# Performance work log

Measured on AMD Instinct MI355X. Metric: run time of the kernel, lower is better.

The kernel has to match this reference:

```python
import jax, jax.numpy as jnp
import numpy as np

N = 100_000   # nodes
E = 1_600_000 # edges
F = 16        # input node features
H = 32        # embedding_size
B = 256       # graphs in batch


def setup_inputs() -> dict:
    key = jax.random.key(0)
    ks = jax.random.split(key, 13)
    s = 0.1  # small init scale for weights
    return {
        "x": jax.random.normal(ks[0], (N, F), jnp.float32),
        "edge_index": jax.random.randint(ks[1], (2, E), 0, N, dtype=jnp.int64),
        "batch_index": jnp.sort(jax.random.randint(ks[2], (N,), 0, B, dtype=jnp.int64)),
        "W0": jax.random.normal(ks[3], (F, H), jnp.float32) * s,
        "b0": jax.random.normal(ks[4], (H,), jnp.float32) * s,
        "W1": jax.random.normal(ks[5], (H, H), jnp.float32) * s,
        "b1": jax.random.normal(ks[6], (H,), jnp.float32) * s,
        "W2": jax.random.normal(ks[7], (H, H), jnp.float32) * s,
        "b2": jax.random.normal(ks[8], (H,), jnp.float32) * s,
        "W3": jax.random.normal(ks[9], (H, H), jnp.float32) * s,
        "b3": jax.random.normal(ks[10], (H, H), jnp.float32)[:, 0] * s,
        "W_out": jax.random.normal(ks[11], (3 * H, 1), jnp.float32) * s,
        "b_out": jax.random.normal(ks[12], (1,), jnp.float32) * s,
    }


def _gcn_forward(x, edge_index, batch_index,
                 W0, b0, W1, b1, W2, b2, W3, b3, W_out, b_out):
    src, dst = edge_index[0], edge_index[1]
    n = x.shape[0]
    # GCN symmetric normalization with self-loops: deg includes the +1 self-loop
    deg = jax.ops.segment_sum(jnp.ones(src.shape[0], x.dtype), dst, num_segments=n) + 1.0
    dinv = jax.lax.rsqrt(deg)
    edge_coef = (dinv[src] * dinv[dst])[:, None]   # [E,1]
    self_coef = (dinv * dinv)[:, None]             # [N,1]

    def conv(h, W, b):
        # x' = D^{-1/2}(A+I)D^{-1/2} (h W) + b  (PyG GCNConv)
        hW = h @ W
        agg = jax.ops.segment_sum(hW[src] * edge_coef, dst, num_segments=n)
        agg = agg + hW * self_coef  # self-loop contribution
        return agg + b

    h = jnp.tanh(conv(x, W0, b0))
    h = jnp.tanh(conv(h, W1, b1))
    h = jnp.tanh(conv(h, W2, b2))
    h = jnp.tanh(conv(h, W3, b3))

    # Global max / mean / add pooling over batch_index
    gmax = jax.ops.segment_max(h, batch_index, num_segments=B)
    gsum = jax.ops.segment_sum(h, batch_index, num_segments=B)
    cnt = jax.ops.segment_sum(jnp.ones(n, h.dtype), batch_index, num_segments=B)
    gmean = gsum / jnp.maximum(cnt, 1.0)[:, None]
    pooled = jnp.concatenate([gmax, gmean, gsum], axis=1)  # [B, 3H]

    out = pooled @ W_out + b_out  # [B, 1]
    return out, pooled


def reference(x, edge_index, batch_index,
              W0, b0, W1, b1, W2, b2, W3, b3, W_out, b_out):
    return _gcn_forward(x, edge_index, batch_index,
                        W0, b0, W1, b1, W2, b2, W3, b3, W_out, b_out)
```

## Files before the change

kernel.cpp:

```cpp
#include <hip/hip_runtime.h>
#include <math.h>

#define N_NODES 100000
#define N_EDGES 1600000
#define F_IN    16
#define H_DIM   32
#define B_GRAPHS 256

#define BSHIFT  7
#define BSIZE   128
#define NBUCKET ((N_NODES + BSIZE - 1) / BSIZE)
#define EPB     8192
#define NCHUNK  ((N_EDGES + EPB - 1) / EPB)
#define CAPB    2560
#define CSTRIDE 2944
#define TPAD    (NBUCKET * CSTRIDE)
#define CURSTR  16
#define NPB     16
#define LAYER_BLOCKS (N_NODES / NPB)

__device__ inline float bf_lo(unsigned u) { return __uint_as_float(u << 16); }
__device__ inline float bf_hi(unsigned u) { return __uint_as_float(u & 0xffff0000u); }
__device__ inline unsigned pack_bf16x2(float a, float b) {
    unsigned ua = __float_as_uint(a), ub = __float_as_uint(b);
    ua += 0x7fffu + ((ua >> 16) & 1u);
    ub += 0x7fffu + ((ub >> 16) & 1u);
    return (ua >> 16) | (ub & 0xffff0000u);
}

__global__ __launch_bounds__(256) void init_cur_kernel(int* __restrict__ bucket_cur) {
    int b = blockIdx.x * 256 + threadIdx.x;
    if (b < NBUCKET) bucket_cur[b * CURSTR] = b * CAPB;
}

__global__ __launch_bounds__(1024) void passB_kernel(const int* __restrict__ ei,
                                                     int* __restrict__ bucket_cur,
                                                     unsigned* __restrict__ rec_out) {
    __shared__ int hist[NBUCKET];
    __shared__ int gcur[NBUCKET];
    int t = threadIdx.x;
    for (int k = t; k < NBUCKET; k += 1024) hist[k] = 0;
    __syncthreads();

    const int* dst = ei + N_EDGES;
    int base = blockIdx.x * EPB;
    int end  = base + EPB; if (end > N_EDGES) end = N_EDGES;

    for (int e = base + t; e < end; e += 1024) atomicAdd(&hist[dst[e] >> BSHIFT], 1);
    __syncthreads();

    for (int k = t; k < NBUCKET; k += 1024) {
        int h = hist[k];
        gcur[k] = h ? atomicAdd(&bucket_cur[k * CURSTR], h) : 0;
    }
    __syncthreads();

    for (int e = base + t; e < end; e += 1024) {
        int d = dst[e], s = ei[e];
        int bk = d >> BSHIFT;
        int pos = atomicAdd(&gcur[bk], 1);
        rec_out[pos] = (unsigned)s | ((unsigned)(d & (BSIZE - 1)) << 20);
    }
}

__global__ __launch_bounds__(256) void dinv_kernel(const unsigned* __restrict__ rec,
                                                   const int* __restrict__ bucket_cur,
                                                   float* __restrict__ dinv) {
    __shared__ int cnt[BSIZE];
    int t = threadIdx.x, b = blockIdx.x;
    if (t < BSIZE) cnt[t] = 0;
    __syncthreads();
    int e1 = bucket_cur[b * CURSTR];
    for (int e = b * CAPB + t; e < e1; e += 256) atomicAdd(&cnt[rec[e] >> 20], 1);
    __syncthreads();
    int nd = (b << BSHIFT) + t;
    if (t < BSIZE && nd < N_NODES) dinv[nd] = rsqrtf((float)cnt[t] + 1.0f);
}

__global__ __launch_bounds__(256) void passC_kernel(const unsigned* __restrict__ rec,
                                                    const int* __restrict__ bucket_cur,
                                                    const float* __restrict__ dinv,
                                                    int2* __restrict__ row_meta,
                                                    int2* __restrict__ csr) {
    __shared__ unsigned stage[CAPB];
    __shared__ int cnt[BSIZE];
    __shared__ int pds[BSIZE];
    __shared__ int cur[BSIZE];
    __shared__ float sdv[BSIZE];
    int t = threadIdx.x, b = blockIdx.x;
    int node0 = b << BSHIFT;
    int e0 = b * CAPB;
    int n = bucket_cur[b * CURSTR] - e0;
    int pbase = b * CSTRIDE;
    if (t < BSIZE) {
        cnt[t] = 0;
        int nd = node0 + t;
        sdv[t] = (nd < N_NODES) ? dinv[nd] : 0.f;
    }
    __syncthreads();
    for (int k = t; k < n; k += 256) {
        unsigned r = rec[e0 + k];
        stage[k] = r;
        atomicAdd(&cnt[r >> 20], 1);
    }
    __syncthreads();
    int pd = 0;
    if (t < BSIZE) { pd = (cnt[t] + 3) & ~3; pds[t] = pd; }
    __syncthreads();
    for (int off = 1; off < BSIZE; off <<= 1) {
        int v = (t < BSIZE && t >= off) ? pds[t - off] : 0;
        __syncthreads();
        if (t < BSIZE) pds[t] += v;
        __syncthreads();
    }
    if (t < BSIZE) {
        int startp = pbase + pds[t] - pd;
        cur[t] = startp;
        int nd = node0 + t;
        if (nd < N_NODES) {
            row_meta[nd] = make_int2(startp, pd);
            for (int k = startp + cnt[t]; k < startp + pd; ++k)
                csr[k] = make_int2(nd, 0);
        }
    }
    __syncthreads();
    for (int k = t; k < n; k += 256) {
        unsigned r = stage[k];
        int dl = r >> 20;
        int s  = r & 0xFFFFF;
        int pos = atomicAdd(&cur[dl], 1);
        csr[pos] = make_int2(s, __float_as_int(dinv[s] * sdv[dl]));
    }
}

template <int FIN, bool PACKED>
__global__ __launch_bounds__(256) void layer_kernel(
        const void* __restrict__ h_in_v,
        const int2* __restrict__ row_meta,
        const int4* __restrict__ csr4,
        const float* __restrict__ dinv,
        const float* __restrict__ W,
        const float* __restrict__ bias,
        unsigned* __restrict__ h_out) {
    constexpr int STR = FIN + 1;
    __shared__ float sW[FIN * H_DIM];
    __shared__ float sb[H_DIM];
    __shared__ float agg[NPB][STR];
    int t = threadIdx.x;
    for (int k = t; k < FIN * H_DIM; k += 256) sW[k] = W[k];
    if (t < H_DIM) sb[t] = bias[t];

    int nl = t >> 4, ln = t & 15;
    int i = blockIdx.x * NPB + nl;
    int2 m = row_meta[i];
    float di = dinv[i], di2 = di * di;
    int q    = m.x >> 1;
    int qend = (m.x + m.y) >> 1;

    if (PACKED) {
        const unsigned* hp = (const unsigned*)h_in_v;
        unsigned u = hp[i * 16 + ln];
        float acc0 = bf_lo(u) * di2, acc1 = bf_hi(u) * di2;
        for (; q + 8 <= qend; q += 8) {
            int4 ca[8];
#pragma unroll
            for (int k = 0; k < 8; ++k) ca[k] = csr4[q + k];
            unsigned v[16];
#pragma unroll
            for (int k = 0; k < 8; ++k) {
                v[2 * k]     = hp[ca[k].x * 16 + ln];
                v[2 * k + 1] = hp[ca[k].z * 16 + ln];
            }
#pragma unroll
            for (int k = 0; k < 8; ++k) {
                float c0 = __int_as_float(ca[k].y), c1 = __int_as_float(ca[k].w);
                acc0 += bf_lo(v[2 * k]) * c0 + bf_lo(v[2 * k + 1]) * c1;
                acc1 += bf_hi(v[2 * k]) * c0 + bf_hi(v[2 * k + 1]) * c1;
            }
        }
        if (q + 4 <= qend) {
            int4 ca[4];
#pragma unroll
            for (int k = 0; k < 4; ++k) ca[k] = csr4[q + k];
#pragma unroll
            for (int k = 0; k < 4; ++k) {
                unsigned v0 = hp[ca[k].x * 16 + ln], v1 = hp[ca[k].z * 16 + ln];
                float c0 = __int_as_float(ca[k].y), c1 = __int_as_float(ca[k].w);
                acc0 += bf_lo(v0) * c0 + bf_lo(v1) * c1;
                acc1 += bf_hi(v0) * c0 + bf_hi(v1) * c1;
            }
            q += 4;
        }
        if (q < qend) {
            int4 a = csr4[q], b = csr4[q + 1];
            unsigned v0 = hp[a.x * 16 + ln], v1 = hp[a.z * 16 + ln];
            unsigned v2 = hp[b.x * 16 + ln], v3 = hp[b.z * 16 + ln];
            float c0 = __int_as_float(a.y), c1 = __int_as_float(a.w);
            float c2 = __int_as_float(b.y), c3 = __int_as_float(b.w);
            acc0 += bf_lo(v0) * c0 + bf_lo(v1) * c1 + bf_lo(v2) * c2 + bf_lo(v3) * c3;
            acc1 += bf_hi(v0) * c0 + bf_hi(v1) * c1 + bf_hi(v2) * c2 + bf_hi(v3) * c3;
        }
        agg[nl][2 * ln]     = acc0;
        agg[nl][2 * ln + 1] = acc1;
    } else {
        const float* xf = (const float*)h_in_v;
        float acc = xf[i * F_IN + ln] * di2;
        for (; q + 8 <= qend; q += 8) {
            int4 ca[8];
#pragma unroll
            for (int k = 0; k < 8; ++k) ca[k] = csr4[q + k];
            float v[16];
#pragma unroll
            for (int k = 0; k < 8; ++k) {
                v[2 * k]     = xf[ca[k].x * F_IN + ln];
                v[2 * k + 1] = xf[ca[k].z * F_IN + ln];
            }
#pragma unroll
            for (int k = 0; k < 8; ++k)
                acc += v[2 * k] * __int_as_float(ca[k].y)
                     + v[2 * k + 1] * __int_as_float(ca[k].w);
        }
        if (q + 4 <= qend) {
            int4 ca[4];
#pragma unroll
            for (int k = 0; k < 4; ++k) ca[k] = csr4[q + k];
#pragma unroll
            for (int k = 0; k < 4; ++k)
                acc += xf[ca[k].x * F_IN + ln] * __int_as_float(ca[k].y)
                     + xf[ca[k].z * F_IN + ln] * __int_as_float(ca[k].w);
            q += 4;
        }
        if (q < qend) {
            int4 a = csr4[q], b = csr4[q + 1];
            acc += xf[a.x * F_IN + ln] * __int_as_float(a.y)
                 + xf[a.z * F_IN + ln] * __int_as_float(a.w)
                 + xf[b.x * F_IN + ln] * __int_as_float(b.y)
                 + xf[b.z * F_IN + ln] * __int_as_float(b.w);
        }
        agg[nl][ln] = acc;
    }
    __syncthreads();

    int j0 = 2 * ln;
    float o0 = sb[j0], o1 = sb[j0 + 1];
    const float* arow = &agg[nl][0];
#pragma unroll
    for (int k = 0; k < FIN; ++k) {
        float a = arow[k];
        o0 += a * sW[k * H_DIM + j0];
        o1 += a * sW[k * H_DIM + j0 + 1];
    }
    h_out[i * 16 + ln] = pack_bf16x2(tanhf(o0), tanhf(o1));
}

__global__ __launch_bounds__(256) void pool_kernel(const unsigned* __restrict__ hp,
                                                   const int* __restrict__ batch,
                                                   const float* __restrict__ Wout,
                                                   const float* __restrict__ bout,
                                                   float* __restrict__ out) {
    int b = blockIdx.x;
    int t = threadIdx.x;
    int lane_n = t >> 5;
    int j = t & 31;

    int lo = 0, hi = N_NODES;
    while (lo < hi) { int mid = (lo + hi) >> 1; if (batch[mid] < b) lo = mid + 1; else hi = mid; }
    int start = lo;
    hi = N_NODES;
    while (lo < hi) { int mid = (lo + hi) >> 1; if (batch[mid] < b + 1) lo = mid + 1; else hi = mid; }
    int end = lo;

    float vmax = -INFINITY, vsum = 0.f;
    for (int i = start + lane_n; i < end; i += 8) {
        unsigned q = hp[i * 16 + (j >> 1)];
        float v = (j & 1) ? bf_hi(q) : bf_lo(q);
        vmax = fmaxf(vmax, v);
        vsum += v;
    }

    __shared__ float smax[8][32];
    __shared__ float ssum[8][32];
    __shared__ float pool96[96];
    smax[lane_n][j] = vmax;
    ssum[lane_n][j] = vsum;
    __syncthreads();

    if (t < 32) {
        float m = smax[0][t], s = ssum[0][t];
#pragma unroll
        for (int n = 1; n < 8; ++n) { m = fmaxf(m, smax[n][t]); s += ssum[n][t]; }
        int cnt = end - start;
        float mean = s / fmaxf((float)cnt, 1.0f);
        pool96[t]      = m;
        pool96[32 + t] = mean;
        pool96[64 + t] = s;
    }
    __syncthreads();

    if (t < 96) out[B_GRAPHS + b * 96 + t] = pool96[t];

    __shared__ float dotbuf[96];
    if (t < 96) dotbuf[t] = pool96[t] * Wout[t];
    __syncthreads();
    if (t == 0) {
        float acc = 0.f;
#pragma unroll
        for (int k = 0; k < 96; ++k) acc += dotbuf[k];
        out[b] = acc + bout[0];
    }
}

extern "C" void kernel_launch(void* const* d_in, const int* in_sizes, int n_in,
                              void* d_out, int out_size, void* d_ws, size_t ws_size,
                              hipStream_t stream) {
    const float* x     = (const float*)d_in[0];
    const int*   ei    = (const int*)  d_in[1];
    const int*   batch = (const int*)  d_in[2];
    const float* W0    = (const float*)d_in[3];
    const float* b0    = (const float*)d_in[4];
    const float* W1    = (const float*)d_in[5];
    const float* b1    = (const float*)d_in[6];
    const float* W2    = (const float*)d_in[7];
    const float* b2    = (const float*)d_in[8];
    const float* W3    = (const float*)d_in[9];
    const float* b3    = (const float*)d_in[10];
    const float* Wout  = (const float*)d_in[11];
    const float* bout  = (const float*)d_in[12];
    float* out = (float*)d_out;

    char* p = (char*)d_ws;
    float*    dinv       = (float*)p;    p += (size_t)N_NODES * 4;
    unsigned* hA         = (unsigned*)p; p += (size_t)N_NODES * 16 * 4;
    unsigned* rec        = (unsigned*)p; p += (size_t)NBUCKET * CAPB * 4;
    int2*     csr        = (int2*)p;     p += (size_t)TPAD * 8;
    int2*     row_meta   = (int2*)p;     p += (size_t)N_NODES * 8;
    int*      bucket_cur = (int*)p;      p += (size_t)NBUCKET * CURSTR * 4;
    unsigned* hB = rec;

    init_cur_kernel<<<(NBUCKET + 255) / 256, 256, 0, stream>>>(bucket_cur);
    passB_kernel<<<NCHUNK, 1024, 0, stream>>>(ei, bucket_cur, rec);
    dinv_kernel<<<NBUCKET, 256, 0, stream>>>(rec, bucket_cur, dinv);
    passC_kernel<<<NBUCKET, 256, 0, stream>>>(rec, bucket_cur, dinv, row_meta, csr);

    layer_kernel<F_IN, false><<<LAYER_BLOCKS, 256, 0, stream>>>(
        x,  row_meta, (const int4*)csr, dinv, W0, b0, hA);
    layer_kernel<H_DIM, true><<<LAYER_BLOCKS, 256, 0, stream>>>(
        hA, row_meta, (const int4*)csr, dinv, W1, b1, hB);
    layer_kernel<H_DIM, true><<<LAYER_BLOCKS, 256, 0, stream>>>(
        hB, row_meta, (const int4*)csr, dinv, W2, b2, hA);
    layer_kernel<H_DIM, true><<<LAYER_BLOCKS, 256, 0, stream>>>(
        hA, row_meta, (const int4*)csr, dinv, W3, b3, hB);

    pool_kernel<<<B_GRAPHS, 256, 0, stream>>>(hB, batch, Wout, bout, out);
}
```

Baseline: 261.5 us.

## Fuse pooling into last GCN layer and compute degrees via global atomics

Removes the separate dinv kernel by counting in-degrees with global atomics during edge bucketing and computing rsqrt inline in passC. The last layer now reduces each 16-node block's tanh outputs per graph in shared memory and pushes max (via order-preserving uint encoding), sum and count to global atomics. A tiny single-block head kernel then finishes mean, writes the pooled output and does the output dot product. This cuts a kernel launch, the binary searches and the pool re-read of h, in exchange for 1.6M extra global atomics on deg and atomic contention on per-graph accumulators, with non-deterministic float sum order.

```diff
diff --git a/kernel.cpp b/kernel.cpp
--- a/kernel.cpp
+++ b/kernel.cpp
@@ -27,15 +27,31 @@
     ub += 0x7fffu + ((ub >> 16) & 1u);
     return (ua >> 16) | (ub & 0xffff0000u);
 }
-
-__global__ __launch_bounds__(256) void init_cur_kernel(int* __restrict__ bucket_cur) {
-    int b = blockIdx.x * 256 + threadIdx.x;
-    if (b < NBUCKET) bucket_cur[b * CURSTR] = b * CAPB;
+__device__ inline unsigned fenc(float f) {
+    unsigned u = __float_as_uint(f);
+    return (u & 0x80000000u) ? ~u : (u | 0x80000000u);
+}
+__device__ inline float fdec(unsigned k) {
+    if (k == 0u) return -INFINITY;
+    return __uint_as_float((k & 0x80000000u) ? (k ^ 0x80000000u) : ~k);
+}
+
+__global__ __launch_bounds__(256) void init_kernel(int* __restrict__ bucket_cur,
+                                                   int* __restrict__ deg,
+                                                   unsigned* __restrict__ gmaxk,
+                                                   float* __restrict__ gsum,
+                                                   int* __restrict__ gcnt) {
+    int t = blockIdx.x * 256 + threadIdx.x;
+    if (t < NBUCKET) bucket_cur[t * CURSTR] = t * CAPB;
+    if (t < N_NODES) deg[t] = 0;
+    if (t < B_GRAPHS * H_DIM) { gmaxk[t] = 0u; gsum[t] = 0.f; }
+    if (t < B_GRAPHS) gcnt[t] = 0;
 }
 
 __global__ __launch_bounds__(1024) void passB_kernel(const int* __restrict__ ei,
                                                      int* __restrict__ bucket_cur,
-                                                     unsigned* __restrict__ rec_out) {
+                                                     unsigned* __restrict__ rec_out,
+                                                     int* __restrict__ deg) {
     __shared__ int hist[NBUCKET];
     __shared__ int gcur[NBUCKET];
     int t = threadIdx.x;
@@ -46,7 +62,11 @@
     int base = blockIdx.x * EPB;
     int end  = base + EPB; if (end > N_EDGES) end = N_EDGES;
 
-    for (int e = base + t; e < end; e += 1024) atomicAdd(&hist[dst[e] >> BSHIFT], 1);
+    for (int e = base + t; e < end; e += 1024) {
+        int d = dst[e];
+        atomicAdd(&hist[d >> BSHIFT], 1);
+        atomicAdd(&deg[d], 1);
+    }
     __syncthreads();
 
     for (int k = t; k < NBUCKET; k += 1024) {
@@ -63,25 +83,12 @@
     }
 }
 
-__global__ __launch_bounds__(256) void dinv_kernel(const unsigned* __restrict__ rec,
-                                                   const int* __restrict__ bucket_cur,
-                                                   float* __restrict__ dinv) {
-    __shared__ int cnt[BSIZE];
-    int t = threadIdx.x, b = blockIdx.x;
-    if (t < BSIZE) cnt[t] = 0;
-    __syncthreads();
-    int e1 = bucket_cur[b * CURSTR];
-    for (int e = b * CAPB + t; e < e1; e += 256) atomicAdd(&cnt[rec[e] >> 20], 1);
-    __syncthreads();
-    int nd = (b << BSHIFT) + t;
-    if (t < BSIZE && nd < N_NODES) dinv[nd] = rsqrtf((float)cnt[t] + 1.0f);
-}
-
 __global__ __launch_bounds__(256) void passC_kernel(const unsigned* __restrict__ rec,
                                                     const int* __restrict__ bucket_cur,
-                                                    const float* __restrict__ dinv,
+                                                    const int* __restrict__ deg,
                                                     int2* __restrict__ row_meta,
-                                                    int2* __restrict__ csr) {
+                                                    int2* __restrict__ csr,
+                                                    float* __restrict__ dinv) {
     __shared__ unsigned stage[CAPB];
     __shared__ int cnt[BSIZE];
     __shared__ int pds[BSIZE];
@@ -95,7 +102,7 @@
     if (t < BSIZE) {
         cnt[t] = 0;
         int nd = node0 + t;
-        sdv[t] = (nd < N_NODES) ? dinv[nd] : 0.f;
+        sdv[t] = (nd < N_NODES) ? rsqrtf((float)deg[nd] + 1.0f) : 0.f;
     }
     __syncthreads();
     for (int k = t; k < n; k += 256) {
@@ -119,6 +126,7 @@
         int nd = node0 + t;
         if (nd < N_NODES) {
             row_meta[nd] = make_int2(startp, pd);
+            dinv[nd] = sdv[t];
             for (int k = startp + cnt[t]; k < startp + pd; ++k)
                 csr[k] = make_int2(nd, 0);
         }
@@ -129,11 +137,12 @@
         int dl = r >> 20;
         int s  = r & 0xFFFFF;
         int pos = atomicAdd(&cur[dl], 1);
-        csr[pos] = make_int2(s, __float_as_int(dinv[s] * sdv[dl]));
-    }
-}
-
-template <int FIN, bool PACKED>
+        float ds = rsqrtf((float)deg[s] + 1.0f);
+        csr[pos] = make_int2(s, __float_as_int(ds * sdv[dl]));
+    }
+}
+
+template <int FIN, bool PACKED, bool POOL>
 __global__ __launch_bounds__(256) void layer_kernel(
         const void* __restrict__ h_in_v,
         const int2* __restrict__ row_meta,
@@ -141,11 +150,16 @@
         const float* __restrict__ dinv,
         const float* __restrict__ W,
         const float* __restrict__ bias,
-        unsigned* __restrict__ h_out) {
+        unsigned* __restrict__ h_out,
+        const int* __restrict__ batch,
+        unsigned* __restrict__ gmaxk,
+        float* __restrict__ gsum,
+        int* __restrict__ gcnt) {
     constexpr int STR = FIN + 1;
     __shared__ float sW[FIN * H_DIM];
     __shared__ float sb[H_DIM];
     __shared__ float agg[NPB][STR];
+    __shared__ int sg[NPB];
     int t = threadIdx.x;
     for (int k = t; k < FIN * H_DIM; k += 256) sW[k] = W[k];
     if (t < H_DIM) sb[t] = bias[t];
@@ -250,64 +264,63 @@
         o0 += a * sW[k * H_DIM + j0];
         o1 += a * sW[k * H_DIM + j0 + 1];
     }
-    h_out[i * 16 + ln] = pack_bf16x2(tanhf(o0), tanhf(o1));
-}
-
-__global__ __launch_bounds__(256) void pool_kernel(const unsigned* __restrict__ hp,
-                                                   const int* __restrict__ batch,
+    float t0 = tanhf(o0), t1 = tanhf(o1);
+
+    if (!POOL) {
+        h_out[i * 16 + ln] = pack_bf16x2(t0, t1);
+    } else {
+        __syncthreads();
+        agg[nl][j0]     = t0;
+        agg[nl][j0 + 1] = t1;
+        if (t < NPB) sg[t] = batch[blockIdx.x * NPB + t];
+        __syncthreads();
+        if (t < H_DIM) {
+            int j = t;
+            int g = sg[0];
+            float mx = agg[0][j], sm = mx;
+            int run = 1;
+            for (int nn = 1; nn < NPB; ++nn) {
+                float v = agg[nn][j];
+                if (sg[nn] != g) {
+                    atomicMax(&gmaxk[g * H_DIM + j], fenc(mx));
+                    atomicAdd(&gsum[g * H_DIM + j], sm);
+                    if (j == 0) atomicAdd(&gcnt[g], run);
+                    g = sg[nn]; mx = v; sm = v; run = 1;
+                } else {
+                    mx = fmaxf(mx, v); sm += v; ++run;
+                }
+            }
+            atomicMax(&gmaxk[g * H_DIM + j], fenc(mx));
+            atomicAdd(&gsum[g * H_DIM + j], sm);
+            if (j == 0) atomicAdd(&gcnt[g], run);
+        }
+    }
+}
+
+__global__ __launch_bounds__(256) void head_kernel(const unsigned* __restrict__ gmaxk,
+                                                   const float* __restrict__ gsum,
+                                                   const int* __restrict__ gcnt,
                                                    const float* __restrict__ Wout,
                                                    const float* __restrict__ bout,
                                                    float* __restrict__ out) {
-    int b = blockIdx.x;
-    int t = threadIdx.x;
-    int lane_n = t >> 5;
-    int j = t & 31;
-
-    int lo = 0, hi = N_NODES;
-    while (lo < hi) { int mid = (lo + hi) >> 1; if (batch[mid] < b) lo = mid + 1; else hi = mid; }
-    int start = lo;
-    hi = N_NODES;
-    while (lo < hi) { int mid = (lo + hi) >> 1; if (batch[mid] < b + 1) lo = mid + 1; else hi = mid; }
-    int end = lo;
-
-    float vmax = -INFINITY, vsum = 0.f;
-    for (int i = start + lane_n; i < end; i += 8) {
-        unsigned q = hp[i * 16 + (j >> 1)];
-        float v = (j & 1) ? bf_hi(q) : bf_lo(q);
-        vmax = fmaxf(vmax, v);
-        vsum += v;
-    }
-
-    __shared__ float smax[8][32];
-    __shared__ float ssum[8][32];
-    __shared__ float pool96[96];
-    smax[lane_n][j] = vmax;
-    ssum[lane_n][j] = vsum;
-    __syncthreads();
-
-    if (t < 32) {
-        float m = smax[0][t], s = ssum[0][t];
-#pragma unroll
-        for (int n = 1; n < 8; ++n) { m = fmaxf(m, smax[n][t]); s += ssum[n][t]; }
-        int cnt = end - start;
-        float mean = s / fmaxf((float)cnt, 1.0f);
-        pool96[t]      = m;
-        pool96[32 + t] = mean;
-        pool96[64 + t] = s;
-    }
-    __syncthreads();
-
-    if (t < 96) out[B_GRAPHS + b * 96 + t] = pool96[t];
-
-    __shared__ float dotbuf[96];
-    if (t < 96) dotbuf[t] = pool96[t] * Wout[t];
-    __syncthreads();
-    if (t == 0) {
-        float acc = 0.f;
-#pragma unroll
-        for (int k = 0; k < 96; ++k) acc += dotbuf[k];
-        out[b] = acc + bout[0];
-    }
+    __shared__ float sWo[3 * H_DIM];
+    int b = threadIdx.x;
+    if (b < 3 * H_DIM) sWo[b] = Wout[b];
+    __syncthreads();
+    float cnt = fmaxf((float)gcnt[b], 1.0f);
+    float acc = 0.f;
+    float* po = out + B_GRAPHS + (size_t)b * 96;
+#pragma unroll
+    for (int j = 0; j < H_DIM; ++j) {
+        float mx = fdec(gmaxk[b * H_DIM + j]);
+        float sm = gsum[b * H_DIM + j];
+        float mean = sm / cnt;
+        po[j]      = mx;
+        po[32 + j] = mean;
+        po[64 + j] = sm;
+        acc += mx * sWo[j] + mean * sWo[32 + j] + sm * sWo[64 + j];
+    }
+    out[b] = acc + bout[0];
 }
 
 extern "C" void kernel_launch(void* const* d_in, const int* in_sizes, int n_in,
@@ -335,21 +348,24 @@
     int2*     csr        = (int2*)p;     p += (size_t)TPAD * 8;
     int2*     row_meta   = (int2*)p;     p += (size_t)N_NODES * 8;
     int*      bucket_cur = (int*)p;      p += (size_t)NBUCKET * CURSTR * 4;
+    int*      deg        = (int*)p;      p += (size_t)N_NODES * 4;
+    unsigned* gmaxk      = (unsigned*)p; p += (size_t)B_GRAPHS * H_DIM * 4;
+    float*    gsumA      = (float*)p;    p += (size_t)B_GRAPHS * H_DIM * 4;
+    int*      gcnt       = (int*)p;      p += (size_t)B_GRAPHS * 4;
     unsigned* hB = rec;
 
-    init_cur_kernel<<<(NBUCKET + 255) / 256, 256, 0, stream>>>(bucket_cur);
-    passB_kernel<<<NCHUNK, 1024, 0, stream>>>(ei, bucket_cur, rec);
-    dinv_kernel<<<NBUCKET, 256, 0, stream>>>(rec, bucket_cur, dinv);
-    passC_kernel<<<NBUCKET, 256, 0, stream>>>(rec, bucket_cur, dinv, row_meta, csr);
-
-    layer_kernel<F_IN, false><<<LAYER_BLOCKS, 256, 0, stream>>>(
-        x,  row_meta, (const int4*)csr, dinv, W0, b0, hA);
-    layer_kernel<H_DIM, true><<<LAYER_BLOCKS, 256, 0, stream>>>(
-        hA, row_meta, (const int4*)csr, dinv, W1, b1, hB);
-    layer_kernel<H_DIM, true><<<LAYER_BLOCKS, 256, 0, stream>>>(
-        hB, row_meta, (const int4*)csr, dinv, W2, b2, hA);
-    layer_kernel<H_DIM, true><<<LAYER_BLOCKS, 256, 0, stream>>>(
-        hA, row_meta, (const int4*)csr, dinv, W3, b3, hB);
-
-    pool_kernel<<<B_GRAPHS, 256, 0, stream>>>(hB, batch, Wout, bout, out);
-}
+    init_kernel<<<(N_NODES + 255) / 256, 256, 0, stream>>>(bucket_cur, deg, gmaxk, gsumA, gcnt);
+    passB_kernel<<<NCHUNK, 1024, 0, stream>>>(ei, bucket_cur, rec, deg);
+    passC_kernel<<<NBUCKET, 256, 0, stream>>>(rec, bucket_cur, deg, row_meta, csr, dinv);
+
+    layer_kernel<F_IN, false, false><<<LAYER_BLOCKS, 256, 0, stream>>>(
+        x,  row_meta, (const int4*)csr, dinv, W0, b0, hA, nullptr, nullptr, nullptr, nullptr);
+    layer_kernel<H_DIM, true, false><<<LAYER_BLOCKS, 256, 0, stream>>>(
+        hA, row_meta, (const int4*)csr, dinv, W1, b1, hB, nullptr, nullptr, nullptr, nullptr);
+    layer_kernel<H_DIM, true, false><<<LAYER_BLOCKS, 256, 0, stream>>>(
+        hB, row_meta, (const int4*)csr, dinv, W2, b2, hA, nullptr, nullptr, nullptr, nullptr);
+    layer_kernel<H_DIM, true, true><<<LAYER_BLOCKS, 256, 0, stream>>>(
+        hA, row_meta, (const int4*)csr, dinv, W3, b3, hB, batch, gmaxk, gsumA, gcnt);
+
+    head_kernel<<<1, 256, 0, stream>>>(gmaxk, gsumA, gcnt, Wout, bout, out);
+}
```

Result: slower. 328.1 us (+25.5%).
